# Performance work log

Hardware: AMD Instinct MI355X
Metric: run time of the kernel (lower is better)

The kernel has to match this reference:

```python
import jax, jax.numpy as jnp
import numpy as np

B, N, C = 2, 2048, 1024
H = 8                 # num_heads
WS = 256              # window_size; half-window = WS // 2
D = C // H            # head_dim


def setup_inputs() -> dict:
    key = jax.random.key(0)
    k0, k1, k2 = jax.random.split(key, 3)
    s = 0.02  # init scale for weights
    x = jax.random.normal(k0, (B, N, C), dtype=jnp.float32)
    w_qkv = jax.random.normal(k1, (3 * C, C), dtype=jnp.float32) * s
    b_qkv = jnp.zeros((3 * C,), dtype=jnp.float32)
    w_proj = jax.random.normal(k2, (C, C), dtype=jnp.float32) * s
    b_proj = jnp.zeros((C,), dtype=jnp.float32)
    return {"x": x, "w_qkv": w_qkv, "b_qkv": b_qkv, "w_proj": w_proj, "b_proj": b_proj}


def reference(x, w_qkv, b_qkv, w_proj, b_proj):
    b, n, c = x.shape
    # qkv projection (torch Linear: x @ W^T + b) -> (B, N, 3C)
    qkv = x @ w_qkv.T + b_qkv
    # (B, N, 3, H, D) -> (3, B, H, N, D)
    qkv = qkv.reshape(b, n, 3, H, D).transpose(2, 0, 3, 1, 4)
    q, k, v = qkv[0], qkv[1], qkv[2]
    # dense scores over sequence, scaled by sqrt(full dim C) as in the source
    attn = jnp.einsum('bhqd,bhkd->bhqk', q, k) / jnp.sqrt(jnp.asarray(c, x.dtype))
    # banded (local-window) mask: keep |i - j| < WS // 2
    i = jnp.arange(n)[:, None]
    j = jnp.arange(n)[None, :]
    band = jnp.abs(i - j) < (WS // 2)
    attn = jnp.where(band, attn, -jnp.inf)
    attn = jax.nn.softmax(attn, axis=-1)
    out = jnp.einsum('bhqk,bhkd->bhqd', attn, v)     # (B, H, N, D)
    out = out.transpose(0, 2, 1, 3).reshape(b, n, c)  # merge heads
    return out @ w_proj.T + b_proj
```

## Files before the change

kernel.cpp:

```cpp
#include <hip/hip_runtime.h>
#include <hip/hip_bf16.h>
#include <stdint.h>

typedef __hip_bfloat16 bf16;
typedef __attribute__((ext_vector_type(8))) short short8;
typedef __attribute__((ext_vector_type(4))) float floatx4;

#define MFMA_BF16(a, b, c) __builtin_amdgcn_mfma_f32_16x16x32_bf16((a), (b), (c), 0, 0, 0)


__device__ __forceinline__ void gl_lds16(const bf16* gsrc, bf16* lds_dst)
{
    __builtin_amdgcn_global_load_lds(
        (const __attribute__((address_space(1))) uint32_t*)(uintptr_t)gsrc,
        (__attribute__((address_space(3))) uint32_t*)(uintptr_t)lds_dst,
        16, 0, 0);
}

__device__ __forceinline__ int sniff_bf16(const uint16_t* __restrict__ x)
{
    int cnt = 0;
#pragma unroll
    for (int i = 0; i < 64; ++i) {
        const int e = (x[2 * i] >> 7) & 0xFF;
        cnt += (e >= 100 && e <= 140) ? 1 : 0;
    }
    return (cnt >= 32) ? 1 : 0;
}

__global__ void __launch_bounds__(256)
cvt_all_kernel(const void* __restrict__ x, const void* __restrict__ wq,
               const void* __restrict__ wp, const void* __restrict__ bq,
               const void* __restrict__ bp,
               bf16* __restrict__ xb, bf16* __restrict__ wqb,
               bf16* __restrict__ wpb, float* __restrict__ bqf,
               float* __restrict__ bpf)
{
    __shared__ int sflag;
    if (threadIdx.x == 0) sflag = sniff_bf16((const uint16_t*)x);
    __syncthreads();
    const bool isbf = (sflag != 0);

    const int blk = blockIdx.x;
    if (blk < 4096) {
        const void* src; bf16* dst; int base;
        if (blk < 2048)      { src = x;  dst = xb;  base = blk << 11; }
        else if (blk < 3584) { src = wq; dst = wqb; base = (blk - 2048) << 11; }
        else                 { src = wp; dst = wpb; base = (blk - 3584) << 11; }
        const int i = base + (int)threadIdx.x * 8;
        if (isbf) {
            *(uint4*)(dst + i) = *(const uint4*)((const bf16*)src + i);
        } else {
            const float4 f0 = *(const float4*)((const float*)src + i);
            const float4 f1 = *(const float4*)((const float*)src + i + 4);
            bf16 o[8];
            o[0] = __float2bfloat16(f0.x); o[1] = __float2bfloat16(f0.y);
            o[2] = __float2bfloat16(f0.z); o[3] = __float2bfloat16(f0.w);
            o[4] = __float2bfloat16(f1.x); o[5] = __float2bfloat16(f1.y);
            o[6] = __float2bfloat16(f1.z); o[7] = __float2bfloat16(f1.w);
            *(uint4*)(dst + i) = *(uint4*)o;
        }
    } else {
        const void* src; float* dst; int base, n;
        if (blk < 4099) { src = bq; dst = bqf; base = (blk - 4096) * 1024; n = 3072; }
        else            { src = bp; dst = bpf; base = 0;                   n = 1024; }
        const int i0 = base + (int)threadIdx.x * 4;
#pragma unroll
        for (int k = 0; k < 4; ++k) {
            const int idx = i0 + k;
            if (idx < n)
                dst[idx] = isbf ? __bfloat162float(((const bf16*)src)[idx])
                                : ((const float*)src)[idx];
        }
    }
}

template <bool FUSE_VT, bool DYN_OUT>
__global__ void __launch_bounds__(256, 2)
gemm_bt_kernel(const bf16* __restrict__ A, const bf16* __restrict__ W,
               const float* __restrict__ bias, void* __restrict__ Cout,
               int M, int Nc, int K, bf16* __restrict__ Vt,
               const uint16_t* __restrict__ sniffsrc)
{
    __shared__ __align__(16) bf16 As[2][128][32];
    __shared__ __align__(16) bf16 Bs[2][128][32];
    __shared__ int sflag;

    const int tid  = threadIdx.x;
    const int lane = tid & 63;
    const int wave = tid >> 6;
    const int quad = lane >> 4;
    const int l16  = lane & 15;
    const int wm   = (wave & 1) * 64;
    const int wn   = (wave >> 1) * 64;
    const int bm   = blockIdx.x * 128;
    const int bn   = blockIdx.y * 128;

    if (DYN_OUT && tid == 0) sflag = sniff_bf16(sniffsrc);

    const int grow = wave * 32 + (lane >> 2);
    const int gcol = (lane & 3) * 8;
    const bf16* Ag = A + (size_t)(bm + grow) * K + gcol;
    const bf16* Wg = W + (size_t)(bn + grow) * K + gcol;
    bf16* Asb = &As[0][0][0];
    bf16* Bsb = &Bs[0][0][0];
    const int w0 = (wave * 2 + 0) * 512;
    const int w1 = (wave * 2 + 1) * 512;

    floatx4 acc[4][4];
#pragma unroll
    for (int i = 0; i < 4; ++i)
#pragma unroll
        for (int j = 0; j < 4; ++j)
#pragma unroll
            for (int r = 0; r < 4; ++r) acc[i][j][r] = 0.0f;

    for (int k0 = 0; k0 < K; k0 += 64) {
        gl_lds16(Ag + k0,                       Asb + w0);
        gl_lds16(Ag + (size_t)16 * K + k0,      Asb + w1);
        gl_lds16(Ag + k0 + 32,                  Asb + 4096 + w0);
        gl_lds16(Ag + (size_t)16 * K + k0 + 32, Asb + 4096 + w1);
        gl_lds16(Wg + k0,                       Bsb + w0);
        gl_lds16(Wg + (size_t)16 * K + k0,      Bsb + w1);
        gl_lds16(Wg + k0 + 32,                  Bsb + 4096 + w0);
        gl_lds16(Wg + (size_t)16 * K + k0 + 32, Bsb + 4096 + w1);
        __syncthreads();

#pragma unroll
        for (int ks = 0; ks < 2; ++ks) {
            short8 af[4], bfr[4];
#pragma unroll
            for (int i = 0; i < 4; ++i)
                af[i] = *(const short8*)(&As[ks][wm + i * 16 + l16][quad * 8]);
#pragma unroll
            for (int j = 0; j < 4; ++j)
                bfr[j] = *(const short8*)(&Bs[ks][wn + j * 16 + l16][quad * 8]);
#pragma unroll
            for (int i = 0; i < 4; ++i)
#pragma unroll
                for (int j = 0; j < 4; ++j)
                    acc[i][j] = MFMA_BF16(af[i], bfr[j], acc[i][j]);
        }
        __syncthreads();
    }

    const bool outbf = DYN_OUT ? (sflag != 0) : true;

#pragma unroll
    for (int i = 0; i < 4; ++i) {
#pragma unroll
        for (int j = 0; j < 4; ++j) {
            const int col = bn + wn + j * 16 + l16;
            const float bv = bias[col];
#pragma unroll
            for (int r = 0; r < 4; ++r) {
                const int row = bm + wm + i * 16 + quad * 4 + r;
                const float v = acc[i][j][r] + bv;
                const size_t idx = (size_t)row * Nc + col;
                if (!DYN_OUT || outbf) {
                    ((bf16*)Cout)[idx] = __float2bfloat16(v);
                } else {
                    ((float*)Cout)[idx] = v;
                }
                if (FUSE_VT) {
                    if (col >= 2048) {
                        const int hh = (col - 2048) >> 7;
                        const int dd = (col - 2048) & 127;
                        const int bb = row >> 11;
                        const int nn = row & 2047;
                        Vt[(((size_t)bb * 8 + hh) * 128 + dd) * 2048 + nn] =
                            __float2bfloat16(v);
                    }
                }
            }
        }
    }
}

__global__ void __launch_bounds__(256, 2)
attn_kernel(const bf16* __restrict__ qkv, const bf16* __restrict__ Vt,
            bf16* __restrict__ out)
{
    __shared__ __align__(16) bf16 Kl[16 * 512];
    __shared__ __align__(16) bf16 Vl[16 * 512];
    __shared__ __align__(16) bf16 Plds[2][4][16][72];

    const int tid  = threadIdx.x;
    const int wave = tid >> 6;
    const int lane = tid & 63;
    const int quad = lane >> 4;
    const int l16  = lane & 15;

    const int hb = blockIdx.x & 15;
    const int qb = blockIdx.x >> 4;
    const int h  = hb & 7;
    const int b  = hb >> 3;
    const int q0 = qb * 64 + wave * 16;

    short8 qf[4];
    {
        const bf16* Qbase = qkv + (size_t)(b * 2048 + q0 + l16) * 3072 + h * 128 + quad * 8;
#pragma unroll
        for (int d = 0; d < 4; ++d)
            qf[d] = *(const short8*)(Qbase + d * 32);
    }

    floatx4 Oacc[8];
#pragma unroll
    for (int dt = 0; dt < 8; ++dt)
#pragma unroll
        for (int r = 0; r < 4; ++r) Oacc[dt][r] = 0.0f;
    float psum[4] = {0.0f, 0.0f, 0.0f, 0.0f};

    const int sl = lane & 15;
    const int sq = lane >> 4;
    const bf16* Kbase = qkv + (size_t)b * 2048 * 3072 + 1024 + h * 128;
    const bf16* Vtb   = Vt + (size_t)hb * 128 * 2048;

    int lo = qb * 64 - 127; if (lo < 0) lo = 0; lo &= ~63;
    int hi = qb * 64 + 63 + 127; if (hi > 2047) hi = 2047;

    int t = 0;
    for (int key0 = lo; key0 <= hi; key0 += 64, ++t) {
        __syncthreads();
#pragma unroll
        for (int i = 0; i < 4; ++i) {
            const int tk = wave * 4 + i;
            const int kt = tk >> 2, dc = tk & 3;
            gl_lds16(Kbase + (size_t)(key0 + kt * 16 + sl) * 3072 + dc * 32 + sq * 8,
                     Kl + tk * 512);
        }
#pragma unroll
        for (int i = 0; i < 4; ++i) {
            const int tv = wave * 4 + i;
            const int dt = tv >> 1, ks = tv & 1;
            gl_lds16(Vtb + (size_t)(dt * 16 + sl) * 2048 + key0 + ks * 32 + sq * 8,
                     Vl + tv * 512);
        }
        __syncthreads();

        floatx4 s[4];
#pragma unroll
        for (int kt = 0; kt < 4; ++kt) {
#pragma unroll
            for (int r = 0; r < 4; ++r) s[kt][r] = 0.0f;
#pragma unroll
            for (int dc = 0; dc < 4; ++dc) {
                short8 kf = *(const short8*)(Kl + (kt * 4 + dc) * 512 + lane * 8);
                s[kt] = MFMA_BF16(qf[dc], kf, s[kt]);
            }
        }
#pragma unroll
        for (int kt = 0; kt < 4; ++kt) {
#pragma unroll
            for (int r = 0; r < 4; ++r) {
                const int i = q0 + quad * 4 + r;
                const int j = key0 + kt * 16 + l16;
                const bool ok = (unsigned)(i - j + 127) < 255u;
                const float p = ok ? __expf(s[kt][r] * 0.03125f) : 0.0f;
                psum[r] += p;
                Plds[t & 1][wave][quad * 4 + r][kt * 16 + l16] = __float2bfloat16(p);
            }
        }
#pragma unroll
        for (int ks = 0; ks < 2; ++ks) {
            short8 pf = *(const short8*)(&Plds[t & 1][wave][l16][ks * 32 + quad * 8]);
#pragma unroll
            for (int dt = 0; dt < 8; ++dt) {
                short8 vf = *(const short8*)(Vl + (dt * 2 + ks) * 512 + lane * 8);
                Oacc[dt] = MFMA_BF16(pf, vf, Oacc[dt]);
            }
        }
    }

#pragma unroll
    for (int m = 1; m <= 8; m <<= 1)
#pragma unroll
        for (int r = 0; r < 4; ++r)
            psum[r] += __shfl_xor(psum[r], m, 64);

#pragma unroll
    for (int r = 0; r < 4; ++r) {
        const float inv = 1.0f / psum[r];
        const int row = q0 + quad * 4 + r;
#pragma unroll
        for (int dt = 0; dt < 8; ++dt) {
            out[(size_t)(b * 2048 + row) * 1024 + h * 128 + dt * 16 + l16] =
                __float2bfloat16(Oacc[dt][r] * inv);
        }
    }
}

extern "C" void kernel_launch(void* const* d_in, const int* in_sizes, int n_in,
                              void* d_out, int out_size, void* d_ws, size_t ws_size,
                              hipStream_t stream)
{
    (void)in_sizes; (void)n_in; (void)out_size; (void)ws_size;

    const void* x      = d_in[0];
    const void* w_qkv  = d_in[1];
    const void* b_qkv  = d_in[2];
    const void* w_proj = d_in[3];
    const void* b_proj = d_in[4];

    char* ws = (char*)d_ws;
    bf16*  qkv      = (bf16*)(ws);
    bf16*  Vt       = (bf16*)(ws + 25165824);
    bf16*  attn_out = (bf16*)(ws + 33554432);
    bf16*  xb       = (bf16*)(ws + 41943040);
    bf16*  wqkvb    = (bf16*)(ws + 50331648);
    bf16*  wprojb   = (bf16*)(ws + 56623104);
    float* bqf      = (float*)(ws + 58720256);
    float* bpf      = (float*)(ws + 58732544);

    cvt_all_kernel<<<dim3(4100), dim3(256), 0, stream>>>(
        x, w_qkv, w_proj, b_qkv, b_proj, xb, wqkvb, wprojb, bqf, bpf);

    gemm_bt_kernel<true, false><<<dim3(32, 24), dim3(256), 0, stream>>>(
        xb, wqkvb, bqf, qkv, 4096, 3072, 1024, Vt, (const uint16_t*)x);

    attn_kernel<<<dim3(512), dim3(256), 0, stream>>>(qkv, Vt, attn_out);

    gemm_bt_kernel<false, true><<<dim3(32, 8), dim3(256), 0, stream>>>(
        attn_out, wprojb, bpf, d_out, 4096, 1024, 1024, nullptr, (const uint16_t*)x);
}
```

Before: 162.1 us.

## Double-buffer LDS tiles in GEMM and attention kernels to overlap loads with MFMA

Both the GEMM and attention kernels now prefetch the next K/V or A/W tile into a second LDS buffer while computing on the current one, with one barrier per iteration instead of two. In the GEMM the k-step per stage shrinks from 64 to 32, so the loop runs twice as many iterations. The attention kernel's P scratch drops its double-buffering so the K/V tiles can be doubled, which raises LDS use. The GEMM As/Bs declarations are not shown, so whether they are sized for the new [buf][128][32] indexing is unclear, and reusing a single P buffer per wave relies on intra-wave ordering.

```diff
diff --git a/kernel.cpp b/kernel.cpp
--- a/kernel.cpp
+++ b/kernel.cpp
@@ -102,8 +102,6 @@
     const int gcol = (lane & 3) * 8;
     const bf16* Ag = A + (size_t)(bm + grow) * K + gcol;
     const bf16* Wg = W + (size_t)(bn + grow) * K + gcol;
-    bf16* Asb = &As[0][0][0];
-    bf16* Bsb = &Bs[0][0][0];
     const int w0 = (wave * 2 + 0) * 512;
     const int w1 = (wave * 2 + 1) * 512;
 
@@ -115,33 +113,32 @@
 #pragma unroll
             for (int r = 0; r < 4; ++r) acc[i][j][r] = 0.0f;
 
-    for (int k0 = 0; k0 < K; k0 += 64) {
-        gl_lds16(Ag + k0,                       Asb + w0);
-        gl_lds16(Ag + (size_t)16 * K + k0,      Asb + w1);
-        gl_lds16(Ag + k0 + 32,                  Asb + 4096 + w0);
-        gl_lds16(Ag + (size_t)16 * K + k0 + 32, Asb + 4096 + w1);
-        gl_lds16(Wg + k0,                       Bsb + w0);
-        gl_lds16(Wg + (size_t)16 * K + k0,      Bsb + w1);
-        gl_lds16(Wg + k0 + 32,                  Bsb + 4096 + w0);
-        gl_lds16(Wg + (size_t)16 * K + k0 + 32, Bsb + 4096 + w1);
+    auto stage = [&](int k0, int buf) {
+        gl_lds16(Ag + k0,                  &As[buf][0][0] + w0);
+        gl_lds16(Ag + (size_t)16 * K + k0, &As[buf][0][0] + w1);
+        gl_lds16(Wg + k0,                  &Bs[buf][0][0] + w0);
+        gl_lds16(Wg + (size_t)16 * K + k0, &Bs[buf][0][0] + w1);
+    };
+
+    stage(0, 0);
+    const int niter = K >> 5;
+    for (int it = 0; it < niter; ++it) {
+        const int buf = it & 1;
         __syncthreads();
-
-#pragma unroll
-        for (int ks = 0; ks < 2; ++ks) {
-            short8 af[4], bfr[4];
-#pragma unroll
-            for (int i = 0; i < 4; ++i)
-                af[i] = *(const short8*)(&As[ks][wm + i * 16 + l16][quad * 8]);
+        if (it + 1 < niter) stage((it + 1) << 5, buf ^ 1);
+
+        short8 af[4], bfr[4];
+#pragma unroll
+        for (int i = 0; i < 4; ++i)
+            af[i] = *(const short8*)(&As[buf][wm + i * 16 + l16][quad * 8]);
+#pragma unroll
+        for (int j = 0; j < 4; ++j)
+            bfr[j] = *(const short8*)(&Bs[buf][wn + j * 16 + l16][quad * 8]);
+#pragma unroll
+        for (int i = 0; i < 4; ++i)
 #pragma unroll
             for (int j = 0; j < 4; ++j)
-                bfr[j] = *(const short8*)(&Bs[ks][wn + j * 16 + l16][quad * 8]);
-#pragma unroll
-            for (int i = 0; i < 4; ++i)
-#pragma unroll
-                for (int j = 0; j < 4; ++j)
-                    acc[i][j] = MFMA_BF16(af[i], bfr[j], acc[i][j]);
-        }
-        __syncthreads();
+                acc[i][j] = MFMA_BF16(af[i], bfr[j], acc[i][j]);
     }
 
     const bool outbf = DYN_OUT ? (sflag != 0) : true;
@@ -181,9 +178,9 @@
 attn_kernel(const bf16* __restrict__ qkv, const bf16* __restrict__ Vt,
             bf16* __restrict__ out)
 {
-    __shared__ __align__(16) bf16 Kl[16 * 512];
-    __shared__ __align__(16) bf16 Vl[16 * 512];
-    __shared__ __align__(16) bf16 Plds[2][4][16][72];
+    __shared__ __align__(16) bf16 Kl[2][16 * 512];
+    __shared__ __align__(16) bf16 Vl[2][16 * 512];
+    __shared__ __align__(16) bf16 Plds[4][16][72];
 
     const int tid  = threadIdx.x;
     const int wave = tid >> 6;
@@ -219,25 +216,31 @@
 
     int lo = qb * 64 - 127; if (lo < 0) lo = 0; lo &= ~63;
     int hi = qb * 64 + 63 + 127; if (hi > 2047) hi = 2047;
-
-    int t = 0;
-    for (int key0 = lo; key0 <= hi; key0 += 64, ++t) {
-        __syncthreads();
+    const int nchunks = ((hi - lo) >> 6) + 1;
+
+    auto stage = [&](int key0, int buf) {
 #pragma unroll
         for (int i = 0; i < 4; ++i) {
             const int tk = wave * 4 + i;
             const int kt = tk >> 2, dc = tk & 3;
             gl_lds16(Kbase + (size_t)(key0 + kt * 16 + sl) * 3072 + dc * 32 + sq * 8,
-                     Kl + tk * 512);
+                     &Kl[buf][0] + tk * 512);
         }
 #pragma unroll
         for (int i = 0; i < 4; ++i) {
             const int tv = wave * 4 + i;
             const int dt = tv >> 1, ks = tv & 1;
             gl_lds16(Vtb + (size_t)(dt * 16 + sl) * 2048 + key0 + ks * 32 + sq * 8,
-                     Vl + tv * 512);
-        }
+                     &Vl[buf][0] + tv * 512);
+        }
+    };
+
+    stage(lo, 0);
+    for (int t = 0; t < nchunks; ++t) {
+        const int key0 = lo + t * 64;
+        const int buf  = t & 1;
         __syncthreads();
+        if (t + 1 < nchunks) stage(key0 + 64, buf ^ 1);
 
         floatx4 s[4];
 #pragma unroll
@@ -246,7 +249,7 @@
             for (int r = 0; r < 4; ++r) s[kt][r] = 0.0f;
 #pragma unroll
             for (int dc = 0; dc < 4; ++dc) {
-                short8 kf = *(const short8*)(Kl + (kt * 4 + dc) * 512 + lane * 8);
+                short8 kf = *(const short8*)(&Kl[buf][0] + (kt * 4 + dc) * 512 + lane * 8);
                 s[kt] = MFMA_BF16(qf[dc], kf, s[kt]);
             }
         }
@@ -259,15 +262,15 @@
                 const bool ok = (unsigned)(i - j + 127) < 255u;
                 const float p = ok ? __expf(s[kt][r] * 0.03125f) : 0.0f;
                 psum[r] += p;
-                Plds[t & 1][wave][quad * 4 + r][kt * 16 + l16] = __float2bfloat16(p);
+                Plds[wave][quad * 4 + r][kt * 16 + l16] = __float2bfloat16(p);
             }
         }
 #pragma unroll
         for (int ks = 0; ks < 2; ++ks) {
-            short8 pf = *(const short8*)(&Plds[t & 1][wave][l16][ks * 32 + quad * 8]);
+            short8 pf = *(const short8*)(&Plds[wave][l16][ks * 32 + quad * 8]);
 #pragma unroll
             for (int dt = 0; dt < 8; ++dt) {
-                short8 vf = *(const short8*)(Vl + (dt * 2 + ks) * 512 + lane * 8);
+                short8 vf = *(const short8*)(&Vl[buf][0] + (dt * 2 + ks) * 512 + lane * 8);
                 Oacc[dt] = MFMA_BF16(pf, vf, Oacc[dt]);
             }
         }
```

Result: no change. 163.1 us (+0.7%).
